# Kernel tuning notes

Hardware: AMD Instinct MI355X
Metric: run time of the kernel (lower is better)

The kernel has to match this reference:

```python
import jax, jax.numpy as jnp
import numpy as np

DIM = 256
N_HEADS = 2
HEAD_DIM = DIM // N_HEADS
SCALE = HEAD_DIM ** -0.5


def setup_inputs() -> dict:
    key = jax.random.key(0)
    ks = jax.random.split(key, 5)
    x = jax.random.normal(ks[0], (8, 4096, 4, DIM), dtype=jnp.float32)
    qkv_w = jax.random.normal(ks[1], (3 * DIM, DIM), dtype=jnp.float32) * (DIM ** -0.5)
    qkv_b = jnp.zeros((3 * DIM,), dtype=jnp.float32)
    out_w = jax.random.normal(ks[2], (DIM, DIM), dtype=jnp.float32) * (DIM ** -0.5)
    out_b = jnp.zeros((DIM,), dtype=jnp.float32)
    ln_g = jnp.ones((DIM,), dtype=jnp.float32)
    ln_b = jnp.zeros((DIM,), dtype=jnp.float32)
    return {"x": x, "qkv_w": qkv_w, "qkv_b": qkv_b, "out_w": out_w,
            "out_b": out_b, "ln_g": ln_g, "ln_b": ln_b}


def reference(x, qkv_w, qkv_b, out_w, out_b, ln_g, ln_b):
    B, N, four, C = x.shape
    H, hd = N_HEADS, HEAD_DIM
    x_flat = x.reshape(B * N, four, C)            # (G, 4, C)
    # LayerNorm over last dim (eps matches torch default 1e-5)
    mu = jnp.mean(x_flat, axis=-1, keepdims=True)
    var = jnp.mean(jnp.square(x_flat - mu), axis=-1, keepdims=True)
    x_n = (x_flat - mu) * jax.lax.rsqrt(var + 1e-5) * ln_g + ln_b
    # QKV projection (torch Linear: y = x @ W.T + b)
    qkv = x_n @ qkv_w.T + qkv_b                   # (G, 4, 3C)
    qkv = qkv.reshape(B * N, four, 3, H, hd)
    q = qkv[:, :, 0].transpose(0, 2, 1, 3)        # (G, H, 4, hd)
    k = qkv[:, :, 1].transpose(0, 2, 1, 3)
    v = qkv[:, :, 2].transpose(0, 2, 1, 3)
    attn = jnp.einsum('ghqd,ghkd->ghqk', q, k) * SCALE
    attn = jax.nn.softmax(attn, axis=-1)
    o = jnp.einsum('ghqk,ghkd->ghqd', attn, v)    # (G, H, 4, hd)
    o = o.transpose(0, 2, 1, 3).reshape(B * N, four, C)
    return x_flat + (o @ out_w.T + out_b)         # (B*N, 4, C)
```

## Files before the change

### kernel.cpp

```cpp
#include <hip/hip_runtime.h>
#include <cstdint>
#include <cstddef>


typedef __attribute__((ext_vector_type(8))) short short8;
typedef __attribute__((ext_vector_type(8))) unsigned short ushort8;
typedef __attribute__((ext_vector_type(16))) float floatx16;

#define DIM    256
#define HD     128
#define ROWS   32
#define XN_S   264
#define QKV_SF 812
#define NT32_QKV 24
#define NT32_OP  8
#define KS16     16
#define SCALE  0.08838834764831845f

__device__ unsigned short g_qkvw[NT32_QKV * KS16 * 64 * 8];
__device__ unsigned short g_outw[NT32_OP * KS16 * 64 * 8];

__device__ __forceinline__ unsigned short f2bf(float f) {
  unsigned int u = __builtin_bit_cast(unsigned int, f);
  u += 0x7fffu + ((u >> 16) & 1u);
  return (unsigned short)(u >> 16);
}
__device__ __forceinline__ float bf2f(unsigned short h) {
  return __builtin_bit_cast(float, (unsigned int)h << 16);
}
__device__ __forceinline__ int swz(int c) { return c + ((c >> 6) << 2); }

__global__ __launch_bounds__(256) void convert_weights(
    const float* __restrict__ qkv_w, const float* __restrict__ out_w) {
  const int id = blockIdx.x * 256 + threadIdx.x;
  const float* src;
  unsigned short* dh;
  if (id < NT32_QKV * KS16 * 64) {
    const int nt = id >> 10, ks = (id >> 6) & 15, lane = id & 63;
    src = qkv_w + (size_t)(nt * 32 + (lane & 31)) * DIM + ks * 16 + (lane >> 5) * 8;
    dh = g_qkvw + (size_t)id * 8;
  } else {
    const int id2 = id - NT32_QKV * KS16 * 64;
    const int nt = id2 >> 10, ks = (id2 >> 6) & 15, lane = id2 & 63;
    src = out_w + (size_t)(nt * 32 + (lane & 31)) * DIM + ks * 16 + (lane >> 5) * 8;
    dh = g_outw + (size_t)id2 * 8;
  }
  float4 a = *reinterpret_cast<const float4*>(src);
  float4 b = *reinterpret_cast<const float4*>(src + 4);
  ushort8 oh;
  oh[0] = f2bf(a.x); oh[1] = f2bf(a.y); oh[2] = f2bf(a.z); oh[3] = f2bf(a.w);
  oh[4] = f2bf(b.x); oh[5] = f2bf(b.y); oh[6] = f2bf(b.z); oh[7] = f2bf(b.w);
  *reinterpret_cast<ushort8*>(dh) = oh;
}

__global__ __launch_bounds__(512, 2) void fused_group_attn(
    const float* __restrict__ x,
    const float* __restrict__ qkv_b, const float* __restrict__ out_b,
    const float* __restrict__ ln_g, const float* __restrict__ ln_b,
    float* __restrict__ out) {
  __shared__ __align__(16) unsigned short xn_hi[ROWS * XN_S];
  __shared__ __align__(16) unsigned short xn_lo[ROWS * XN_S];
  __shared__ __align__(16) float qkvf[ROWS * QKV_SF];

  const int tid  = threadIdx.x;
  const int lane = tid & 63;
  const int wid  = tid >> 6;
  const int l31  = lane & 31;
  const int khalf = lane >> 5;
  const size_t rowbase = (size_t)blockIdx.x * ROWS;

  {
    const int row = tid >> 4;
    const int seg = tid & 15;
    const float4* xr4 = reinterpret_cast<const float4*>(
        x + (rowbase + row) * DIM + seg * 16);
    float4 v[4];
    float s = 0.f, sq = 0.f;
#pragma unroll
    for (int i = 0; i < 4; ++i) {
      v[i] = xr4[i];
      s  += v[i].x + v[i].y + v[i].z + v[i].w;
      sq += v[i].x * v[i].x + v[i].y * v[i].y + v[i].z * v[i].z + v[i].w * v[i].w;
    }
#pragma unroll
    for (int off = 1; off < 16; off <<= 1) {
      s  += __shfl_xor(s, off);
      sq += __shfl_xor(sq, off);
    }
    const float mu   = s * (1.f / DIM);
    const float var  = sq * (1.f / DIM) - mu * mu;
    const float rstd = rsqrtf(var + 1e-5f);
    const float4* g4 = reinterpret_cast<const float4*>(ln_g + seg * 16);
    const float4* b4 = reinterpret_cast<const float4*>(ln_b + seg * 16);
#pragma unroll
    for (int p = 0; p < 2; ++p) {
      float4 ga = g4[2 * p], gb = g4[2 * p + 1];
      float4 ba = b4[2 * p], bb = b4[2 * p + 1];
      float4 va = v[2 * p],  vb = v[2 * p + 1];
      float n[8] = {
        (va.x - mu) * rstd * ga.x + ba.x, (va.y - mu) * rstd * ga.y + ba.y,
        (va.z - mu) * rstd * ga.z + ba.z, (va.w - mu) * rstd * ga.w + ba.w,
        (vb.x - mu) * rstd * gb.x + bb.x, (vb.y - mu) * rstd * gb.y + bb.y,
        (vb.z - mu) * rstd * gb.z + bb.z, (vb.w - mu) * rstd * gb.w + bb.w};
      ushort8 oh, ol;
#pragma unroll
      for (int e = 0; e < 8; ++e) {
        unsigned short h = f2bf(n[e]);
        oh[e] = h;
        ol[e] = f2bf(n[e] - bf2f(h));
      }
      *reinterpret_cast<ushort8*>(&xn_hi[row * XN_S + seg * 16 + p * 8]) = oh;
      *reinterpret_cast<ushort8*>(&xn_lo[row * XN_S + seg * 16 + p * 8]) = ol;
    }
  }
  __syncthreads();

  {
    floatx16 acc[3];
#pragma unroll
    for (int n = 0; n < 3; ++n)
#pragma unroll
      for (int i = 0; i < 16; ++i) acc[n][i] = 0.f;
#pragma unroll
    for (int ks = 0; ks < KS16; ++ks) {
      const int aoff = ks * 16 + khalf * 8;
      short8 ah = *reinterpret_cast<const short8*>(&xn_hi[l31 * XN_S + aoff]);
      short8 al = *reinterpret_cast<const short8*>(&xn_lo[l31 * XN_S + aoff]);
#pragma unroll
      for (int n = 0; n < 3; ++n) {
        const int boff = (((wid * 3 + n) * KS16 + ks) * 64 + lane) * 8;
        short8 bh = *reinterpret_cast<const short8*>(g_qkvw + boff);
        acc[n] = __builtin_amdgcn_mfma_f32_32x32x16_bf16(ah, bh, acc[n], 0, 0, 0);
        acc[n] = __builtin_amdgcn_mfma_f32_32x32x16_bf16(al, bh, acc[n], 0, 0, 0);
      }
    }
#pragma unroll
    for (int n = 0; n < 3; ++n) {
      const int col = (wid * 3 + n) * 32 + l31;
      const int scol = swz(col);
      const float bias = qkv_b[col];
#pragma unroll
      for (int i = 0; i < 16; ++i) {
        const int row = (i & 3) + 8 * (i >> 2) + 4 * khalf;
        qkvf[row * QKV_SF + scol] = acc[n][i] + bias;
      }
    }
  }

  short8 pb[KS16];
#pragma unroll
  for (int ks = 0; ks < KS16; ++ks)
    pb[ks] = *reinterpret_cast<const short8*>(
        g_outw + (size_t)((wid * KS16 + ks) * 64 + lane) * 8);

  __syncthreads();

  {
    const int g    = wid;
    const int half = lane >> 5;
    const int l5   = lane & 31;
    const int t = (l5 & 15) >> 2, u = l5 & 3, c = l5 >> 4;
    const float4* qp = reinterpret_cast<const float4*>(
        &qkvf[(4 * g + t) * QKV_SF + swz(half * HD + c * 64)]);
    const float4* kp = reinterpret_cast<const float4*>(
        &qkvf[(4 * g + u) * QKV_SF + swz(256 + half * HD + c * 64)]);
    float sdot = 0.f;
#pragma unroll
    for (int j = 0; j < 16; ++j) {
      float4 qv = qp[j];
      float4 kv = kp[j];
      sdot += qv.x * kv.x + qv.y * kv.y + qv.z * kv.z + qv.w * kv.w;
    }
    sdot += __shfl_xor(sdot, 16);
    sdot *= SCALE;
    float mx = fmaxf(sdot, __shfl_xor(sdot, 1));
    mx = fmaxf(mx, __shfl_xor(mx, 2));
    float ex = __expf(sdot - mx);
    float den = ex + __shfl_xor(ex, 1);
    den += __shfl_xor(den, 2);
    const float p = ex / den;

    const int t2 = l5 >> 3, dseg = l5 & 7;
    float o[16];
#pragma unroll
    for (int e = 0; e < 16; ++e) o[e] = 0.f;
#pragma unroll
    for (int uu = 0; uu < 4; ++uu) {
      const float pu = __shfl(p, (lane & 32) + t2 * 4 + uu);
      const float4* vp = reinterpret_cast<const float4*>(
          &qkvf[(4 * g + uu) * QKV_SF + swz(512 + half * HD + dseg * 16)]);
      float4 v0 = vp[0], v1 = vp[1], v2 = vp[2], v3 = vp[3];
      o[0]  += pu * v0.x; o[1]  += pu * v0.y; o[2]  += pu * v0.z; o[3]  += pu * v0.w;
      o[4]  += pu * v1.x; o[5]  += pu * v1.y; o[6]  += pu * v1.z; o[7]  += pu * v1.w;
      o[8]  += pu * v2.x; o[9]  += pu * v2.y; o[10] += pu * v2.z; o[11] += pu * v2.w;
      o[12] += pu * v3.x; o[13] += pu * v3.y; o[14] += pu * v3.z; o[15] += pu * v3.w;
    }
    ushort8 h0, h1, l0, l1;
#pragma unroll
    for (int e = 0; e < 8; ++e) {
      unsigned short ha = f2bf(o[e]);
      h0[e] = ha; l0[e] = f2bf(o[e] - bf2f(ha));
      unsigned short hb = f2bf(o[e + 8]);
      h1[e] = hb; l1[e] = f2bf(o[e + 8] - bf2f(hb));
    }
    const int ooff = (4 * g + t2) * XN_S + half * HD + dseg * 16;
    *reinterpret_cast<ushort8*>(&xn_hi[ooff])     = h0;
    *reinterpret_cast<ushort8*>(&xn_hi[ooff + 8]) = h1;
    *reinterpret_cast<ushort8*>(&xn_lo[ooff])     = l0;
    *reinterpret_cast<ushort8*>(&xn_lo[ooff + 8]) = l1;
  }
  __syncthreads();

  {
    floatx16 acc;
#pragma unroll
    for (int i = 0; i < 16; ++i) acc[i] = 0.f;
#pragma unroll
    for (int ks = 0; ks < KS16; ++ks) {
      const int aoff = ks * 16 + khalf * 8;
      short8 ah = *reinterpret_cast<const short8*>(&xn_hi[l31 * XN_S + aoff]);
      short8 al = *reinterpret_cast<const short8*>(&xn_lo[l31 * XN_S + aoff]);
      acc = __builtin_amdgcn_mfma_f32_32x32x16_bf16(ah, pb[ks], acc, 0, 0, 0);
      acc = __builtin_amdgcn_mfma_f32_32x32x16_bf16(al, pb[ks], acc, 0, 0, 0);
    }
    const int col = wid * 32 + l31;
    const float bias = out_b[col];
#pragma unroll
    for (int i = 0; i < 16; ++i) {
      const int row = (i & 3) + 8 * (i >> 2) + 4 * khalf;
      const size_t gidx = (rowbase + row) * DIM + col;
      out[gidx] = acc[i] + bias + x[gidx];
    }
  }
}

extern "C" void kernel_launch(void* const* d_in, const int* in_sizes, int n_in,
                              void* d_out, int out_size, void* d_ws, size_t ws_size,
                              hipStream_t stream) {
  const float* x     = (const float*)d_in[0];
  const float* qkv_w = (const float*)d_in[1];
  const float* qkv_b = (const float*)d_in[2];
  const float* out_w = (const float*)d_in[3];
  const float* out_b = (const float*)d_in[4];
  const float* ln_g  = (const float*)d_in[5];
  const float* ln_b  = (const float*)d_in[6];
  float* out = (float*)d_out;

  hipLaunchKernelGGL(convert_weights, dim3(128), dim3(256), 0, stream, qkv_w, out_w);

  const int rows = in_sizes[0] / DIM;
  const int nblk = rows / ROWS;
  hipLaunchKernelGGL(fused_group_attn, dim3(nblk), dim3(512), 0, stream,
                     x, qkv_b, out_b, ln_g, ln_b, out);
}
```

Baseline: 362.6 us.

## Process 64 rows per block in two chunks and XOR-swizzle shared memory

Each block now handles 64 rows in two 32-row chunks. Every QKV weight fragment loaded from global memory is reused for two MFMA row tiles, and the out-projection weights held in registers are reused for both chunks. The qkv staging buffer is double-used across chunks, with the attention/out-projection phases interleaved with the second chunk's QKV writeback. Padded layouts are replaced by XOR swizzles to avoid LDS bank conflicts. The extra accumulators raise register pressure, and halving the block count may reduce occupancy or parallelism.

```diff
diff --git a/kernel.cpp b/kernel.cpp
--- a/kernel.cpp
+++ b/kernel.cpp
@@ -9,9 +9,7 @@
 
 #define DIM    256
 #define HD     128
-#define ROWS   32
-#define XN_S   264
-#define QKV_SF 812
+#define ROWS   64
 #define NT32_QKV 24
 #define NT32_OP  8
 #define KS16     16
@@ -28,7 +26,15 @@
 __device__ __forceinline__ float bf2f(unsigned short h) {
   return __builtin_bit_cast(float, (unsigned int)h << 16);
 }
-__device__ __forceinline__ int swz(int c) { return c + ((c >> 6) << 2); }
+__device__ __forceinline__ int xidx(int r, int c) {
+  const int g = c >> 3;
+  return r * 256 + (((g ^ (r & 7)) << 3) | (c & 7));
+}
+__device__ __forceinline__ int qidx(int r, int w) {
+  const int g4 = w >> 2;
+  const int g4s = g4 ^ ((r & 7) ^ (((g4 >> 4) & 3) << 1));
+  return r * 768 + (g4s << 2) + (w & 3);
+}
 
 __global__ __launch_bounds__(256) void convert_weights(
     const float* __restrict__ qkv_w, const float* __restrict__ out_w) {
@@ -58,9 +64,9 @@
     const float* __restrict__ qkv_b, const float* __restrict__ out_b,
     const float* __restrict__ ln_g, const float* __restrict__ ln_b,
     float* __restrict__ out) {
-  __shared__ __align__(16) unsigned short xn_hi[ROWS * XN_S];
-  __shared__ __align__(16) unsigned short xn_lo[ROWS * XN_S];
-  __shared__ __align__(16) float qkvf[ROWS * QKV_SF];
+  __shared__ __align__(16) float qkvf[32 * 768];
+  __shared__ __align__(16) unsigned short xn_hi[ROWS * 256];
+  __shared__ __align__(16) unsigned short xn_lo[ROWS * 256];
 
   const int tid  = threadIdx.x;
   const int lane = tid & 63;
@@ -69,11 +75,13 @@
   const int khalf = lane >> 5;
   const size_t rowbase = (size_t)blockIdx.x * ROWS;
 
-  {
-    const int row = tid >> 4;
+#pragma unroll
+  for (int ch = 0; ch < 2; ++ch) {
+    const int row = (tid >> 4);
+    const int xr  = ch * 32 + row;
     const int seg = tid & 15;
     const float4* xr4 = reinterpret_cast<const float4*>(
-        x + (rowbase + row) * DIM + seg * 16);
+        x + (rowbase + xr) * DIM + seg * 16);
     float4 v[4];
     float s = 0.f, sq = 0.f;
 #pragma unroll
@@ -109,40 +117,46 @@
         oh[e] = h;
         ol[e] = f2bf(n[e] - bf2f(h));
       }
-      *reinterpret_cast<ushort8*>(&xn_hi[row * XN_S + seg * 16 + p * 8]) = oh;
-      *reinterpret_cast<ushort8*>(&xn_lo[row * XN_S + seg * 16 + p * 8]) = ol;
-    }
-  }
-  __syncthreads();
-
+      const int xo = xidx(xr, seg * 16 + p * 8);
+      *reinterpret_cast<ushort8*>(&xn_hi[xo]) = oh;
+      *reinterpret_cast<ushort8*>(&xn_lo[xo]) = ol;
+    }
+  }
+  __syncthreads();
+
+  floatx16 acc1[3];
   {
-    floatx16 acc[3];
+    floatx16 acc0[3];
 #pragma unroll
     for (int n = 0; n < 3; ++n)
 #pragma unroll
-      for (int i = 0; i < 16; ++i) acc[n][i] = 0.f;
+      for (int i = 0; i < 16; ++i) { acc0[n][i] = 0.f; acc1[n][i] = 0.f; }
 #pragma unroll
     for (int ks = 0; ks < KS16; ++ks) {
-      const int aoff = ks * 16 + khalf * 8;
-      short8 ah = *reinterpret_cast<const short8*>(&xn_hi[l31 * XN_S + aoff]);
-      short8 al = *reinterpret_cast<const short8*>(&xn_lo[l31 * XN_S + aoff]);
+      const int xo0 = xidx(l31,      ks * 16 + khalf * 8);
+      const int xo1 = xidx(32 + l31, ks * 16 + khalf * 8);
+      short8 a0h = *reinterpret_cast<const short8*>(&xn_hi[xo0]);
+      short8 a0l = *reinterpret_cast<const short8*>(&xn_lo[xo0]);
+      short8 a1h = *reinterpret_cast<const short8*>(&xn_hi[xo1]);
+      short8 a1l = *reinterpret_cast<const short8*>(&xn_lo[xo1]);
 #pragma unroll
       for (int n = 0; n < 3; ++n) {
         const int boff = (((wid * 3 + n) * KS16 + ks) * 64 + lane) * 8;
         short8 bh = *reinterpret_cast<const short8*>(g_qkvw + boff);
-        acc[n] = __builtin_amdgcn_mfma_f32_32x32x16_bf16(ah, bh, acc[n], 0, 0, 0);
-        acc[n] = __builtin_amdgcn_mfma_f32_32x32x16_bf16(al, bh, acc[n], 0, 0, 0);
+        acc0[n] = __builtin_amdgcn_mfma_f32_32x32x16_bf16(a0h, bh, acc0[n], 0, 0, 0);
+        acc0[n] = __builtin_amdgcn_mfma_f32_32x32x16_bf16(a0l, bh, acc0[n], 0, 0, 0);
+        acc1[n] = __builtin_amdgcn_mfma_f32_32x32x16_bf16(a1h, bh, acc1[n], 0, 0, 0);
+        acc1[n] = __builtin_amdgcn_mfma_f32_32x32x16_bf16(a1l, bh, acc1[n], 0, 0, 0);
       }
     }
 #pragma unroll
     for (int n = 0; n < 3; ++n) {
       const int col = (wid * 3 + n) * 32 + l31;
-      const int scol = swz(col);
       const float bias = qkv_b[col];
 #pragma unroll
       for (int i = 0; i < 16; ++i) {
         const int row = (i & 3) + 8 * (i >> 2) + 4 * khalf;
-        qkvf[row * QKV_SF + scol] = acc[n][i] + bias;
+        qkvf[qidx(row, col)] = acc0[n][i] + bias;
       }
     }
   }
@@ -155,20 +169,19 @@
 
   __syncthreads();
 
-  {
-    const int g    = wid;
+  auto P3 = [&](int ch) {
     const int half = lane >> 5;
     const int l5   = lane & 31;
     const int t = (l5 & 15) >> 2, u = l5 & 3, c = l5 >> 4;
-    const float4* qp = reinterpret_cast<const float4*>(
-        &qkvf[(4 * g + t) * QKV_SF + swz(half * HD + c * 64)]);
-    const float4* kp = reinterpret_cast<const float4*>(
-        &qkvf[(4 * g + u) * QKV_SF + swz(256 + half * HD + c * 64)]);
+    const int rq = 4 * wid + t;
+    const int rk = 4 * wid + u;
     float sdot = 0.f;
 #pragma unroll
     for (int j = 0; j < 16; ++j) {
-      float4 qv = qp[j];
-      float4 kv = kp[j];
+      const float4 qv = *reinterpret_cast<const float4*>(
+          &qkvf[qidx(rq, half * HD + c * 64 + 4 * j)]);
+      const float4 kv = *reinterpret_cast<const float4*>(
+          &qkvf[qidx(rk, 256 + half * HD + c * 64 + 4 * j)]);
       sdot += qv.x * kv.x + qv.y * kv.y + qv.z * kv.z + qv.w * kv.w;
     }
     sdot += __shfl_xor(sdot, 16);
@@ -187,13 +200,16 @@
 #pragma unroll
     for (int uu = 0; uu < 4; ++uu) {
       const float pu = __shfl(p, (lane & 32) + t2 * 4 + uu);
-      const float4* vp = reinterpret_cast<const float4*>(
-          &qkvf[(4 * g + uu) * QKV_SF + swz(512 + half * HD + dseg * 16)]);
-      float4 v0 = vp[0], v1 = vp[1], v2 = vp[2], v3 = vp[3];
-      o[0]  += pu * v0.x; o[1]  += pu * v0.y; o[2]  += pu * v0.z; o[3]  += pu * v0.w;
-      o[4]  += pu * v1.x; o[5]  += pu * v1.y; o[6]  += pu * v1.z; o[7]  += pu * v1.w;
-      o[8]  += pu * v2.x; o[9]  += pu * v2.y; o[10] += pu * v2.z; o[11] += pu * v2.w;
-      o[12] += pu * v3.x; o[13] += pu * v3.y; o[14] += pu * v3.z; o[15] += pu * v3.w;
+      const int rv = 4 * wid + uu;
+#pragma unroll
+      for (int j = 0; j < 4; ++j) {
+        const float4 vv = *reinterpret_cast<const float4*>(
+            &qkvf[qidx(rv, 512 + half * HD + dseg * 16 + 4 * j)]);
+        o[4 * j]     += pu * vv.x;
+        o[4 * j + 1] += pu * vv.y;
+        o[4 * j + 2] += pu * vv.z;
+        o[4 * j + 3] += pu * vv.w;
+      }
     }
     ushort8 h0, h1, l0, l1;
 #pragma unroll
@@ -203,23 +219,24 @@
       unsigned short hb = f2bf(o[e + 8]);
       h1[e] = hb; l1[e] = f2bf(o[e + 8] - bf2f(hb));
     }
-    const int ooff = (4 * g + t2) * XN_S + half * HD + dseg * 16;
-    *reinterpret_cast<ushort8*>(&xn_hi[ooff])     = h0;
-    *reinterpret_cast<ushort8*>(&xn_hi[ooff + 8]) = h1;
-    *reinterpret_cast<ushort8*>(&xn_lo[ooff])     = l0;
-    *reinterpret_cast<ushort8*>(&xn_lo[ooff + 8]) = l1;
-  }
-  __syncthreads();
-
-  {
+    const int orow = ch * 32 + 4 * wid + t2;
+    const int oc   = half * HD + dseg * 16;
+    const int oo0 = xidx(orow, oc), oo1 = xidx(orow, oc + 8);
+    *reinterpret_cast<ushort8*>(&xn_hi[oo0]) = h0;
+    *reinterpret_cast<ushort8*>(&xn_hi[oo1]) = h1;
+    *reinterpret_cast<ushort8*>(&xn_lo[oo0]) = l0;
+    *reinterpret_cast<ushort8*>(&xn_lo[oo1]) = l1;
+  };
+
+  auto P4 = [&](int ch) {
     floatx16 acc;
 #pragma unroll
     for (int i = 0; i < 16; ++i) acc[i] = 0.f;
 #pragma unroll
     for (int ks = 0; ks < KS16; ++ks) {
-      const int aoff = ks * 16 + khalf * 8;
-      short8 ah = *reinterpret_cast<const short8*>(&xn_hi[l31 * XN_S + aoff]);
-      short8 al = *reinterpret_cast<const short8*>(&xn_lo[l31 * XN_S + aoff]);
+      const int xo = xidx(ch * 32 + l31, ks * 16 + khalf * 8);
+      short8 ah = *reinterpret_cast<const short8*>(&xn_hi[xo]);
+      short8 al = *reinterpret_cast<const short8*>(&xn_lo[xo]);
       acc = __builtin_amdgcn_mfma_f32_32x32x16_bf16(ah, pb[ks], acc, 0, 0, 0);
       acc = __builtin_amdgcn_mfma_f32_32x32x16_bf16(al, pb[ks], acc, 0, 0, 0);
     }
@@ -228,10 +245,31 @@
 #pragma unroll
     for (int i = 0; i < 16; ++i) {
       const int row = (i & 3) + 8 * (i >> 2) + 4 * khalf;
-      const size_t gidx = (rowbase + row) * DIM + col;
+      const size_t gidx = (rowbase + ch * 32 + row) * DIM + col;
       out[gidx] = acc[i] + bias + x[gidx];
     }
-  }
+  };
+
+  P3(0);
+  __syncthreads();
+
+#pragma unroll
+  for (int n = 0; n < 3; ++n) {
+    const int col = (wid * 3 + n) * 32 + l31;
+    const float bias = qkv_b[col];
+#pragma unroll
+    for (int i = 0; i < 16; ++i) {
+      const int row = (i & 3) + 8 * (i >> 2) + 4 * khalf;
+      qkvf[qidx(row, col)] = acc1[n][i] + bias;
+    }
+  }
+  P4(0);
+  __syncthreads();
+
+  P3(1);
+  __syncthreads();
+
+  P4(1);
 }
 
 extern "C" void kernel_launch(void* const* d_in, const int* in_sizes, int n_in,
```

Measured after the change: 473.2 us. 30.5% more time.
